# Optimization experiments

Hardware: AMD Instinct MI355X
Metric: run time of the kernel (lower is better)

## Reference

```python
import jax, jax.numpy as jnp
from jax import lax
import numpy as np

B, T, H, IN = 64, 2048, 256, 1


def setup_inputs() -> dict:
    key = jax.random.key(0)
    ks = jax.random.split(key, 12)
    s = 1.0 / np.sqrt(H)  # torch LSTM init scale (use normal*s for simplicity)
    return {
        "x": jax.random.normal(ks[0], (B, T, IN), jnp.float32),
        "Wih0": jax.random.normal(ks[1], (4 * H, IN), jnp.float32) * s,
        "Whh0": jax.random.normal(ks[2], (4 * H, H), jnp.float32) * s,
        "bih0": jax.random.normal(ks[3], (4 * H,), jnp.float32) * s,
        "bhh0": jax.random.normal(ks[4], (4 * H,), jnp.float32) * s,
        "Wih1": jax.random.normal(ks[5], (4 * H, H), jnp.float32) * s,
        "Whh1": jax.random.normal(ks[6], (4 * H, H), jnp.float32) * s,
        "bih1": jax.random.normal(ks[7], (4 * H,), jnp.float32) * s,
        "bhh1": jax.random.normal(ks[8], (4 * H,), jnp.float32) * s,
        "fc_w": jax.random.normal(ks[9], (1, H), jnp.float32) * s,
        "fc_b": jax.random.normal(ks[10], (1,), jnp.float32) * s,
    }


def _lstm_layer(x, Wih, Whh, bih, bhh):
    # x: [B, T, D_in] -> h sequence [B, T, H]; torch gate order (i, f, g, o)
    Bb = x.shape[0]
    Hh = Whh.shape[1]
    # precompute input contribution for all timesteps: [B, T, 4H]
    xg = jnp.einsum('btd,gd->btg', x, Wih) + bih + bhh

    def step(carry, xt):
        h, c = carry
        g = xt + h @ Whh.T  # [B, 4H]
        i, f, gg, o = jnp.split(g, 4, axis=-1)
        i = jax.nn.sigmoid(i)
        f = jax.nn.sigmoid(f)
        gg = jnp.tanh(gg)
        o = jax.nn.sigmoid(o)
        c = f * c + i * gg
        h = o * jnp.tanh(c)
        return (h, c), h

    h0 = jnp.zeros((Bb, Hh), x.dtype)
    c0 = jnp.zeros((Bb, Hh), x.dtype)
    (_, _), hs = lax.scan(step, (h0, c0), jnp.swapaxes(xg, 0, 1))  # hs: [T, B, H]
    return jnp.swapaxes(hs, 0, 1)


def reference(x, Wih0, Whh0, bih0, bhh0, Wih1, Whh1, bih1, bhh1, fc_w, fc_b):
    h1 = _lstm_layer(x, Wih0, Whh0, bih0, bhh0)   # [B, T, H]
    h2 = _lstm_layer(h1, Wih1, Whh1, bih1, bhh1)  # [B, T, H]
    out = jnp.einsum('bth,oh->bto', h2, fc_w) + fc_b  # [B, T, 1]
    return out
```

## Files before the change

kernel.cpp:

```cpp
#include <hip/hip_runtime.h>

#define TT 2048
#define NTHR 512
#define NWG 64

#define ABORT_O 0
#define FL_O    1024
#define H0_O    16384
#define H1_O    (16384 + 2*65536)
#define WS_TOTAL (16384 + 4*65536)

#define A0_HI    0
#define A0_LO    16384
#define AIH_HI   0
#define AIH_LO   16384
#define AHH_HI   32768
#define AHH_LO   49152
#define FWL_O    65536
#define HSH_O    65600
#define SMEM_BYTES 67648

typedef __bf16 bf16;
typedef __bf16 bf16x8 __attribute__((ext_vector_type(8)));
typedef float f32x4 __attribute__((ext_vector_type(4)));
typedef unsigned int u32;
typedef u32 u32x4 __attribute__((ext_vector_type(4)));
typedef unsigned short u16;

__device__ __forceinline__ f32x4 MFMA(bf16x8 a, bf16x8 b, f32x4 c) {
  return __builtin_amdgcn_mfma_f32_16x16x32_bf16(a, b, c, 0, 0, 0);
}
__device__ __forceinline__ float sigf(float v) { return 1.0f / (1.0f + __expf(-v)); }
__device__ __forceinline__ float tanhfast(float x) {
  float e = __expf(2.0f * x);
  return 1.0f - 2.0f / (e + 1.0f);
}
__device__ __forceinline__ u16 bfbits(float f) { return __builtin_bit_cast(u16, (bf16)f); }

__device__ __forceinline__ bf16x8 ld16d(const void* p) {
  u32x4 v;
  asm volatile("global_load_dwordx4 %0, %1, off sc0 sc1" : "=v"(v) : "v"(p));
  return __builtin_bit_cast(bf16x8, v);
}
__device__ __forceinline__ void wait_all_loads() {
  asm volatile("s_waitcnt vmcnt(0)" ::: "memory");
  __builtin_amdgcn_sched_barrier(0);
}
__device__ __forceinline__ void st16d(void* p, u16 h) {
  u32 v = h;
  asm volatile("global_store_short %0, %1, off sc0 sc1" :: "v"(p), "v"(v) : "memory");
}
__device__ __forceinline__ void st32_deep(u32* p, u32 v) {
  asm volatile("global_store_dword %0, %1, off sc0 sc1" :: "v"(p), "v"(v) : "memory");
}
__device__ __forceinline__ u32 ld_deep(const u32* p) {
  u32 v;
  asm volatile("global_load_dword %0, %1, off sc0 sc1\n\ts_waitcnt vmcnt(0)"
               : "=v"(v) : "v"(p) : "memory");
  return v;
}

__device__ __forceinline__ void wait_barrier(const u32* flags, u32 need, u32* abortp) {
  const int lane = threadIdx.x & 63;
  const u32* p = flags + lane * 32;
  int it = 0;
  for (;;) {
    u32 v = ld_deep(p);
    if (__all((int)(v >= need))) break;
    if (((++it) & 63) == 0) {
      u32 ab = ld_deep(abortp);
      if (__any((int)(ab != 0))) break;
      if (it >= (1 << 16)) { if (lane == 0) st32_deep(abortp, 1u); break; }
    }
  }
}

extern "C" __global__ __launch_bounds__(NTHR)
void lstm_persist(const float* __restrict__ x,
                  const float* __restrict__ Wih0, const float* __restrict__ Whh0,
                  const float* __restrict__ bih0, const float* __restrict__ bhh0,
                  const float* __restrict__ Wih1, const float* __restrict__ Whh1,
                  const float* __restrict__ bih1, const float* __restrict__ bhh1,
                  const float* __restrict__ fcw, const float* __restrict__ fcb,
                  float* __restrict__ out, char* __restrict__ ws)
{
  extern __shared__ char smem[];
  const int tid  = threadIdx.x;
  const int slot = blockIdx.x;
  const bool isL1 = slot >= 32;
  const int sl = isL1 ? slot - 32 : slot;

  u32* abortp = (u32*)(ws + ABORT_O);
  u32* flags  = (u32*)(ws + FL_O);

  const int w = tid >> 6, l = tid & 63, lr = l & 15, lk = l >> 4;
  const int rowb = (w & 1) * 16;
  const int colb = (w >> 1) * 16;
  const int b  = colb + lr;
  const int i  = (w & 1) * 4 + lk;
  const int gd = sl * 8 + i;

  if (!isL1) {
    bf16x8* Ahi = (bf16x8*)(smem + A0_HI);
    bf16x8* Alo = (bf16x8*)(smem + A0_LO);
    for (int idx = tid; idx < 1024; idx += NTHR) {
      int r = idx >> 5, kb = idx & 31;
      int grow = (r & 3) * 256 + sl * 8 + (r >> 2);
      const float* src = Whh0 + grow * 256 + kb * 8;
      bf16x8 hi, lo;
#pragma unroll
      for (int e = 0; e < 8; e++) { float v = src[e]; bf16 h = (bf16)v; hi[e] = h; lo[e] = (bf16)(v - (float)h); }
      Ahi[kb * 32 + r] = hi;  Alo[kb * 32 + r] = lo;
    }
  } else {
    bf16x8* AihH = (bf16x8*)(smem + AIH_HI);
    bf16x8* AihL = (bf16x8*)(smem + AIH_LO);
    bf16x8* AhhH = (bf16x8*)(smem + AHH_HI);
    bf16x8* AhhL = (bf16x8*)(smem + AHH_LO);
    for (int idx = tid; idx < 1024; idx += NTHR) {
      int r = idx >> 5, kb = idx & 31;
      int grow = (r & 3) * 256 + sl * 8 + (r >> 2);
      {
        const float* src = Wih1 + grow * 256 + kb * 8;
        bf16x8 hi, lo;
#pragma unroll
        for (int e = 0; e < 8; e++) { float v = src[e]; bf16 h = (bf16)v; hi[e] = h; lo[e] = (bf16)(v - (float)h); }
        AihH[kb * 32 + r] = hi;  AihL[kb * 32 + r] = lo;
      }
      {
        const float* src = Whh1 + grow * 256 + kb * 8;
        bf16x8 hi, lo;
#pragma unroll
        for (int e = 0; e < 8; e++) { float v = src[e]; bf16 h = (bf16)v; hi[e] = h; lo[e] = (bf16)(v - (float)h); }
        AhhH[kb * 32 + r] = hi;  AhhL[kb * 32 + r] = lo;
      }
    }
    if (tid < 8) ((float*)(smem + FWL_O))[tid] = fcw[sl * 8 + tid];
  }

  float wib_r[4], bias_r[4];
#pragma unroll
  for (int g = 0; g < 4; g++) {
    if (!isL1) { wib_r[g] = Wih0[g * 256 + gd]; bias_r[g] = bih0[g * 256 + gd] + bhh0[g * 256 + gd]; }
    else       { wib_r[g] = 0.0f;               bias_r[g] = bih1[g * 256 + gd] + bhh1[g * 256 + gd]; }
  }
  float creg = 0.0f;
  const float fb = fcb[0];
  __syncthreads();

  for (int t = 0; t <= TT; ++t) {
    if (t > 0) {
      if (tid < 64) wait_barrier(flags, (u32)t, abortp);
      __syncthreads();
    }

    if (!isL1) {
      if (t < TT) {
        const char* hp = ws + H0_O + (size_t)((t - 1) & 1) * 65536;
        bf16x8 bh[8], bl[8];
#pragma unroll
        for (int ks = 0; ks < 8; ks++) {
          int kb = ks * 4 + lk;
          const char* p = hp + (size_t)(kb * 64 + b) * 16;
          bh[ks] = ld16d(p);
          bl[ks] = ld16d(p + 32768);
        }
        float xv = x[(size_t)b * TT + t];
        wait_all_loads();

        bf16x8* Ahi = (bf16x8*)(smem + A0_HI);
        bf16x8* Alo = (bf16x8*)(smem + A0_LO);
        f32x4 acc = {0.f, 0.f, 0.f, 0.f};
#pragma unroll
        for (int ks = 0; ks < 8; ks++) {
          int kb = ks * 4 + lk;
          bf16x8 ah = Ahi[kb * 32 + rowb + lr];
          bf16x8 al = Alo[kb * 32 + rowb + lr];
          acc = MFMA(ah, bh[ks], acc);
          acc = MFMA(ah, bl[ks], acc);
          acc = MFMA(al, bh[ks], acc);
        }
        float pi = acc[0] + wib_r[0] * xv + bias_r[0];
        float pf = acc[1] + wib_r[1] * xv + bias_r[1];
        float pg = acc[2] + wib_r[2] * xv + bias_r[2];
        float po = acc[3] + wib_r[3] * xv + bias_r[3];
        float c = sigf(pf) * creg + sigf(pi) * tanhfast(pg);
        creg = c;
        float h = sigf(po) * tanhfast(c);
        u16 hb = bfbits(h);
        u16 lb = bfbits(h - (float)(bf16)h);
        char* wp = ws + H0_O + (size_t)(t & 1) * 65536 + (size_t)(sl * 64 + b) * 16 + i * 2;
        st16d(wp, hb);
        st16d(wp + 32768, lb);
      }
    } else {
      if (t >= 1) {
        const char* h0p = ws + H0_O + (size_t)((t - 1) & 1) * 65536;
        const char* h1p = ws + H1_O + (size_t)(t & 1) * 65536;
        bf16x8 b0h[8], b0l[8], b1h[8], b1l[8];
#pragma unroll
        for (int ks = 0; ks < 8; ks++) {
          int kb = ks * 4 + lk;
          const char* p0 = h0p + (size_t)(kb * 64 + b) * 16;
          const char* p1 = h1p + (size_t)(kb * 64 + b) * 16;
          b0h[ks] = ld16d(p0);  b0l[ks] = ld16d(p0 + 32768);
          b1h[ks] = ld16d(p1);  b1l[ks] = ld16d(p1 + 32768);
        }
        wait_all_loads();

        bf16x8* AihH = (bf16x8*)(smem + AIH_HI);
        bf16x8* AihL = (bf16x8*)(smem + AIH_LO);
        bf16x8* AhhH = (bf16x8*)(smem + AHH_HI);
        bf16x8* AhhL = (bf16x8*)(smem + AHH_LO);
        f32x4 acc = {0.f, 0.f, 0.f, 0.f};
#pragma unroll
        for (int ks = 0; ks < 8; ks++) {
          int kb = ks * 4 + lk;
          bf16x8 aih = AihH[kb * 32 + rowb + lr];
          bf16x8 ail = AihL[kb * 32 + rowb + lr];
          bf16x8 ahh = AhhH[kb * 32 + rowb + lr];
          bf16x8 ahl = AhhL[kb * 32 + rowb + lr];
          acc = MFMA(aih, b0h[ks], acc);
          acc = MFMA(aih, b0l[ks], acc);
          acc = MFMA(ail, b0h[ks], acc);
          acc = MFMA(ahh, b1h[ks], acc);
          acc = MFMA(ahh, b1l[ks], acc);
          acc = MFMA(ahl, b1h[ks], acc);
        }
        float pi = acc[0] + bias_r[0];
        float pf = acc[1] + bias_r[1];
        float pg = acc[2] + bias_r[2];
        float po = acc[3] + bias_r[3];
        float c = sigf(pf) * creg + sigf(pi) * tanhfast(pg);
        creg = c;
        float h = sigf(po) * tanhfast(c);
        u16 hb = bfbits(h);
        u16 lb = bfbits(h - (float)(bf16)h);
        char* wp = ws + H1_O + (size_t)((t - 1) & 1) * 65536 + (size_t)(sl * 64 + b) * 16 + i * 2;
        st16d(wp, hb);
        st16d(wp + 32768, lb);
        ((float*)(smem + HSH_O))[i * 64 + b] = h;
      }
    }

    asm volatile("s_waitcnt vmcnt(0)" ::: "memory");
    __syncthreads();
    if (tid == 0 && t < TT)
      st32_deep(flags + slot * 32, (u32)(t + 1));

    if (isL1 && t >= 1 && tid >= 64 && tid < 128) {
      const float* hsh = (const float*)(smem + HSH_O);
      const float* fwl = (const float*)(smem + FWL_O);
      int bb = tid - 64;
      float acc = 0.0f;
#pragma unroll
      for (int d = 0; d < 8; d++) acc += fwl[d] * hsh[d * 64 + bb];
      if (sl == 0) acc += fb;
      atomicAdd(out + (size_t)bb * TT + (t - 1), acc);
    }
  }
}

extern "C" void kernel_launch(void* const* d_in, const int* in_sizes, int n_in,
                              void* d_out, int out_size, void* d_ws, size_t ws_size,
                              hipStream_t stream) {
  (void)in_sizes; (void)n_in; (void)ws_size;
  hipFuncSetAttribute((const void*)lstm_persist,
                      hipFuncAttributeMaxDynamicSharedMemorySize, SMEM_BYTES);
  hipMemsetAsync(d_ws, 0, WS_TOTAL, stream);
  hipMemsetAsync(d_out, 0, (size_t)out_size * sizeof(float), stream);
  lstm_persist<<<dim3(NWG), dim3(NTHR), SMEM_BYTES, stream>>>(
      (const float*)d_in[0],
      (const float*)d_in[1], (const float*)d_in[2],
      (const float*)d_in[3], (const float*)d_in[4],
      (const float*)d_in[5], (const float*)d_in[6],
      (const float*)d_in[7], (const float*)d_in[8],
      (const float*)d_in[9], (const float*)d_in[10],
      (float*)d_out, (char*)d_ws);
}
```

Measured before the change: 9.152 ms.

## Exchange hidden state as fp32 and split to bf16 hi/lo on the consumer side

Producers now write h as a single 32-bit float store instead of two 16-bit stores of bf16 hi/lo parts. Consumers load two dwordx4 per fragment and rebuild the hi/lo bf16 split in registers before the MFMAs. Barrier flags are packed contiguously instead of padded 128 bytes apart, and MFMAs on the all-zero initial state are skipped. This halves the store count and turns sub-word stores into dword stores, at the price of extra conversion ALU work on the critical path and possible contention on the shared flag cache line.

```diff
diff --git a/kernel.cpp b/kernel.cpp
--- a/kernel.cpp
+++ b/kernel.cpp
@@ -5,7 +5,7 @@
 #define NWG 64
 
 #define ABORT_O 0
-#define FL_O    1024
+#define FL_O    256
 #define H0_O    16384
 #define H1_O    (16384 + 2*65536)
 #define WS_TOTAL (16384 + 4*65536)
@@ -35,20 +35,15 @@
   float e = __expf(2.0f * x);
   return 1.0f - 2.0f / (e + 1.0f);
 }
-__device__ __forceinline__ u16 bfbits(float f) { return __builtin_bit_cast(u16, (bf16)f); }
-
-__device__ __forceinline__ bf16x8 ld16d(const void* p) {
+
+__device__ __forceinline__ u32x4 ld16d(const void* p) {
   u32x4 v;
   asm volatile("global_load_dwordx4 %0, %1, off sc0 sc1" : "=v"(v) : "v"(p));
-  return __builtin_bit_cast(bf16x8, v);
+  return v;
 }
 __device__ __forceinline__ void wait_all_loads() {
   asm volatile("s_waitcnt vmcnt(0)" ::: "memory");
   __builtin_amdgcn_sched_barrier(0);
-}
-__device__ __forceinline__ void st16d(void* p, u16 h) {
-  u32 v = h;
-  asm volatile("global_store_short %0, %1, off sc0 sc1" :: "v"(p), "v"(v) : "memory");
 }
 __device__ __forceinline__ void st32_deep(u32* p, u32 v) {
   asm volatile("global_store_dword %0, %1, off sc0 sc1" :: "v"(p), "v"(v) : "memory");
@@ -60,9 +55,36 @@
   return v;
 }
 
+__device__ __forceinline__ u32 cv_hi(u32 w0, u32 w1) {
+  float f0 = __builtin_bit_cast(float, w0);
+  float f1 = __builtin_bit_cast(float, w1);
+  u16 h0 = __builtin_bit_cast(u16, (bf16)f0);
+  u16 h1 = __builtin_bit_cast(u16, (bf16)f1);
+  return (u32)h0 | ((u32)h1 << 16);
+}
+__device__ __forceinline__ u32 cv_lo(u32 w0, u32 w1) {
+  float f0 = __builtin_bit_cast(float, w0);
+  float f1 = __builtin_bit_cast(float, w1);
+  float r0 = f0 - (float)((bf16)f0);
+  float r1 = f1 - (float)((bf16)f1);
+  u16 l0 = __builtin_bit_cast(u16, (bf16)r0);
+  u16 l1 = __builtin_bit_cast(u16, (bf16)r1);
+  return (u32)l0 | ((u32)l1 << 16);
+}
+
+__device__ __forceinline__ void mk_frags(u32x4 qa, u32x4 qb, bf16x8& bh, bf16x8& bl) {
+  u32x4 ph, pl;
+  ph[0] = cv_hi(qa[0], qa[1]);  pl[0] = cv_lo(qa[0], qa[1]);
+  ph[1] = cv_hi(qa[2], qa[3]);  pl[1] = cv_lo(qa[2], qa[3]);
+  ph[2] = cv_hi(qb[0], qb[1]);  pl[2] = cv_lo(qb[0], qb[1]);
+  ph[3] = cv_hi(qb[2], qb[3]);  pl[3] = cv_lo(qb[2], qb[3]);
+  bh = __builtin_bit_cast(bf16x8, ph);
+  bl = __builtin_bit_cast(bf16x8, pl);
+}
+
 __device__ __forceinline__ void wait_barrier(const u32* flags, u32 need, u32* abortp) {
   const int lane = threadIdx.x & 63;
-  const u32* p = flags + lane * 32;
+  const u32* p = flags + lane;
   int it = 0;
   for (;;) {
     u32 v = ld_deep(p);
@@ -70,7 +92,7 @@
     if (((++it) & 63) == 0) {
       u32 ab = ld_deep(abortp);
       if (__any((int)(ab != 0))) break;
-      if (it >= (1 << 16)) { if (lane == 0) st32_deep(abortp, 1u); break; }
+      if (it >= (1 << 16)) { if (lane == 0) st32_deep((u32*)abortp, 1u); break; }
     }
   }
 }
@@ -88,7 +110,7 @@
   const int tid  = threadIdx.x;
   const int slot = blockIdx.x;
   const bool isL1 = slot >= 32;
-  const int sl = isL1 ? slot - 32 : slot;
+  const int sl = slot & 31;
 
   u32* abortp = (u32*)(ws + ABORT_O);
   u32* flags  = (u32*)(ws + FL_O);
@@ -99,6 +121,7 @@
   const int b  = colb + lr;
   const int i  = (w & 1) * 4 + lk;
   const int gd = sl * 8 + i;
+  const u32 hwi = (u32)(((sl * 2 + (i >> 2)) * 64 + b) * 4 + (i & 3));
 
   if (!isL1) {
     bf16x8* Ahi = (bf16x8*)(smem + A0_HI);
@@ -157,28 +180,30 @@
     if (!isL1) {
       if (t < TT) {
         const char* hp = ws + H0_O + (size_t)((t - 1) & 1) * 65536;
-        bf16x8 bh[8], bl[8];
+        u32x4 qa[8], qb[8];
 #pragma unroll
         for (int ks = 0; ks < 8; ks++) {
           int kb = ks * 4 + lk;
-          const char* p = hp + (size_t)(kb * 64 + b) * 16;
-          bh[ks] = ld16d(p);
-          bl[ks] = ld16d(p + 32768);
+          qa[ks] = ld16d(hp + (size_t)((kb * 2) * 64 + b) * 16);
+          qb[ks] = ld16d(hp + (size_t)((kb * 2 + 1) * 64 + b) * 16);
         }
         float xv = x[(size_t)b * TT + t];
         wait_all_loads();
 
-        bf16x8* Ahi = (bf16x8*)(smem + A0_HI);
-        bf16x8* Alo = (bf16x8*)(smem + A0_LO);
+        const bf16x8* Ahi = (const bf16x8*)(smem + A0_HI);
+        const bf16x8* Alo = (const bf16x8*)(smem + A0_LO);
         f32x4 acc = {0.f, 0.f, 0.f, 0.f};
-#pragma unroll
-        for (int ks = 0; ks < 8; ks++) {
-          int kb = ks * 4 + lk;
-          bf16x8 ah = Ahi[kb * 32 + rowb + lr];
-          bf16x8 al = Alo[kb * 32 + rowb + lr];
-          acc = MFMA(ah, bh[ks], acc);
-          acc = MFMA(ah, bl[ks], acc);
-          acc = MFMA(al, bh[ks], acc);
+        if (t > 0) {
+#pragma unroll
+          for (int ks = 0; ks < 8; ks++) {
+            bf16x8 bh, bl;
+            mk_frags(qa[ks], qb[ks], bh, bl);
+            bf16x8 ah = Ahi[(ks * 4 + lk) * 32 + rowb + lr];
+            bf16x8 al = Alo[(ks * 4 + lk) * 32 + rowb + lr];
+            acc = MFMA(ah, bh, acc);
+            acc = MFMA(ah, bl, acc);
+            acc = MFMA(al, bh, acc);
+          }
         }
         float pi = acc[0] + wib_r[0] * xv + bias_r[0];
         float pf = acc[1] + wib_r[1] * xv + bias_r[1];
@@ -187,45 +212,48 @@
         float c = sigf(pf) * creg + sigf(pi) * tanhfast(pg);
         creg = c;
         float h = sigf(po) * tanhfast(c);
-        u16 hb = bfbits(h);
-        u16 lb = bfbits(h - (float)(bf16)h);
-        char* wp = ws + H0_O + (size_t)(t & 1) * 65536 + (size_t)(sl * 64 + b) * 16 + i * 2;
-        st16d(wp, hb);
-        st16d(wp + 32768, lb);
+        st32_deep((u32*)(ws + H0_O + (size_t)(t & 1) * 65536) + hwi,
+                  __builtin_bit_cast(u32, h));
       }
     } else {
       if (t >= 1) {
         const char* h0p = ws + H0_O + (size_t)((t - 1) & 1) * 65536;
         const char* h1p = ws + H1_O + (size_t)(t & 1) * 65536;
-        bf16x8 b0h[8], b0l[8], b1h[8], b1l[8];
+        u32x4 qa0[8], qb0[8], qa1[8], qb1[8];
 #pragma unroll
         for (int ks = 0; ks < 8; ks++) {
           int kb = ks * 4 + lk;
-          const char* p0 = h0p + (size_t)(kb * 64 + b) * 16;
-          const char* p1 = h1p + (size_t)(kb * 64 + b) * 16;
-          b0h[ks] = ld16d(p0);  b0l[ks] = ld16d(p0 + 32768);
-          b1h[ks] = ld16d(p1);  b1l[ks] = ld16d(p1 + 32768);
+          qa0[ks] = ld16d(h0p + (size_t)((kb * 2) * 64 + b) * 16);
+          qb0[ks] = ld16d(h0p + (size_t)((kb * 2 + 1) * 64 + b) * 16);
+          qa1[ks] = ld16d(h1p + (size_t)((kb * 2) * 64 + b) * 16);
+          qb1[ks] = ld16d(h1p + (size_t)((kb * 2 + 1) * 64 + b) * 16);
         }
         wait_all_loads();
 
-        bf16x8* AihH = (bf16x8*)(smem + AIH_HI);
-        bf16x8* AihL = (bf16x8*)(smem + AIH_LO);
-        bf16x8* AhhH = (bf16x8*)(smem + AHH_HI);
-        bf16x8* AhhL = (bf16x8*)(smem + AHH_LO);
+        const bf16x8* AihH = (const bf16x8*)(smem + AIH_HI);
+        const bf16x8* AihL = (const bf16x8*)(smem + AIH_LO);
+        const bf16x8* AhhH = (const bf16x8*)(smem + AHH_HI);
+        const bf16x8* AhhL = (const bf16x8*)(smem + AHH_LO);
         f32x4 acc = {0.f, 0.f, 0.f, 0.f};
 #pragma unroll
         for (int ks = 0; ks < 8; ks++) {
           int kb = ks * 4 + lk;
+          bf16x8 bh, bl;
+          mk_frags(qa0[ks], qb0[ks], bh, bl);
           bf16x8 aih = AihH[kb * 32 + rowb + lr];
           bf16x8 ail = AihL[kb * 32 + rowb + lr];
-          bf16x8 ahh = AhhH[kb * 32 + rowb + lr];
-          bf16x8 ahl = AhhL[kb * 32 + rowb + lr];
-          acc = MFMA(aih, b0h[ks], acc);
-          acc = MFMA(aih, b0l[ks], acc);
-          acc = MFMA(ail, b0h[ks], acc);
-          acc = MFMA(ahh, b1h[ks], acc);
-          acc = MFMA(ahh, b1l[ks], acc);
-          acc = MFMA(ahl, b1h[ks], acc);
+          acc = MFMA(aih, bh, acc);
+          acc = MFMA(aih, bl, acc);
+          acc = MFMA(ail, bh, acc);
+          if (t >= 2) {
+            bf16x8 ch, cl;
+            mk_frags(qa1[ks], qb1[ks], ch, cl);
+            bf16x8 ahh = AhhH[kb * 32 + rowb + lr];
+            bf16x8 ahl = AhhL[kb * 32 + rowb + lr];
+            acc = MFMA(ahh, ch, acc);
+            acc = MFMA(ahh, cl, acc);
+            acc = MFMA(ahl, ch, acc);
+          }
         }
         float pi = acc[0] + bias_r[0];
         float pf = acc[1] + bias_r[1];
@@ -234,11 +262,8 @@
         float c = sigf(pf) * creg + sigf(pi) * tanhfast(pg);
         creg = c;
         float h = sigf(po) * tanhfast(c);
-        u16 hb = bfbits(h);
-        u16 lb = bfbits(h - (float)(bf16)h);
-        char* wp = ws + H1_O + (size_t)((t - 1) & 1) * 65536 + (size_t)(sl * 64 + b) * 16 + i * 2;
-        st16d(wp, hb);
-        st16d(wp + 32768, lb);
+        st32_deep((u32*)(ws + H1_O + (size_t)((t - 1) & 1) * 65536) + hwi,
+                  __builtin_bit_cast(u32, h));
         ((float*)(smem + HSH_O))[i * 64 + b] = h;
       }
     }
@@ -246,7 +271,7 @@
     asm volatile("s_waitcnt vmcnt(0)" ::: "memory");
     __syncthreads();
     if (tid == 0 && t < TT)
-      st32_deep(flags + slot * 32, (u32)(t + 1));
+      st32_deep(&flags[slot], (u32)(t + 1));
 
     if (isL1 && t >= 1 && tid >= 64 && tid < 128) {
       const float* hsh = (const float*)(smem + HSH_O);
@@ -265,10 +290,10 @@
                               void* d_out, int out_size, void* d_ws, size_t ws_size,
                               hipStream_t stream) {
   (void)in_sizes; (void)n_in; (void)ws_size;
-  hipFuncSetAttribute((const void*)lstm_persist,
-                      hipFuncAttributeMaxDynamicSharedMemorySize, SMEM_BYTES);
-  hipMemsetAsync(d_ws, 0, WS_TOTAL, stream);
-  hipMemsetAsync(d_out, 0, (size_t)out_size * sizeof(float), stream);
+  (void)hipFuncSetAttribute((const void*)lstm_persist,
+                            hipFuncAttributeMaxDynamicSharedMemorySize, SMEM_BYTES);
+  (void)hipMemsetAsync(d_ws, 0, WS_TOTAL, stream);
+  (void)hipMemsetAsync(d_out, 0, (size_t)out_size * sizeof(float), stream);
   lstm_persist<<<dim3(NWG), dim3(NTHR), SMEM_BYTES, stream>>>(
       (const float*)d_in[0],
       (const float*)d_in[1], (const float*)d_in[2],
```

New measurement: 15.85 ms. +73.1%, slower.

## Loosen layer-0 barrier dependency on layer-1 with 4-deep h0 ring buffer

Applied to the files above, without the earlier changes.

Layer-0 workgroups no longer wait on layer-1 progress for the current step. They only require layer-1 flags from two steps back, and h0 now sits in a 4-slot ring so it cannot be overwritten before layer 1 consumes it. This lets layer 0 run ahead and cuts the stalls caused by the lockstep global barrier between the two layers. It also skips MFMAs on known-zero initial hidden states at t=0 for layer 0 and t=1 for layer 1, at the cost of more workspace and a looser ordering argument that must hold for correctness.

```diff
diff --git a/kernel.cpp b/kernel.cpp
--- a/kernel.cpp
+++ b/kernel.cpp
@@ -7,8 +7,8 @@
 #define ABORT_O 0
 #define FL_O    1024
 #define H0_O    16384
-#define H1_O    (16384 + 2*65536)
-#define WS_TOTAL (16384 + 4*65536)
+#define H1_O    (16384 + 4*65536)
+#define WS_TOTAL (16384 + 4*65536 + 2*65536)
 
 #define A0_HI    0
 #define A0_LO    16384
@@ -60,8 +60,10 @@
   return v;
 }
 
-__device__ __forceinline__ void wait_barrier(const u32* flags, u32 need, u32* abortp) {
+__device__ __forceinline__ void wait_barrier(const u32* flags, u32 need_lo, u32 need_hi,
+                                             u32* abortp) {
   const int lane = threadIdx.x & 63;
+  const u32 need = (lane < 32) ? need_lo : need_hi;
   const u32* p = flags + lane * 32;
   int it = 0;
   for (;;) {
@@ -88,7 +90,7 @@
   const int tid  = threadIdx.x;
   const int slot = blockIdx.x;
   const bool isL1 = slot >= 32;
-  const int sl = isL1 ? slot - 32 : slot;
+  const int sl = slot & 31;
 
   u32* abortp = (u32*)(ws + ABORT_O);
   u32* flags  = (u32*)(ws + FL_O);
@@ -150,13 +152,16 @@
 
   for (int t = 0; t <= TT; ++t) {
     if (t > 0) {
-      if (tid < 64) wait_barrier(flags, (u32)t, abortp);
+      if (tid < 64) {
+        u32 need_hi = isL1 ? (u32)t : (t >= 2 ? (u32)(t - 2) : 0u);
+        wait_barrier(flags, (u32)t, need_hi, abortp);
+      }
       __syncthreads();
     }
 
     if (!isL1) {
       if (t < TT) {
-        const char* hp = ws + H0_O + (size_t)((t - 1) & 1) * 65536;
+        const char* hp = ws + H0_O + (size_t)((t + 3) & 3) * 65536;
         bf16x8 bh[8], bl[8];
 #pragma unroll
         for (int ks = 0; ks < 8; ks++) {
@@ -168,17 +173,19 @@
         float xv = x[(size_t)b * TT + t];
         wait_all_loads();
 
-        bf16x8* Ahi = (bf16x8*)(smem + A0_HI);
-        bf16x8* Alo = (bf16x8*)(smem + A0_LO);
+        const bf16x8* Ahi = (const bf16x8*)(smem + A0_HI);
+        const bf16x8* Alo = (const bf16x8*)(smem + A0_LO);
         f32x4 acc = {0.f, 0.f, 0.f, 0.f};
-#pragma unroll
-        for (int ks = 0; ks < 8; ks++) {
-          int kb = ks * 4 + lk;
-          bf16x8 ah = Ahi[kb * 32 + rowb + lr];
-          bf16x8 al = Alo[kb * 32 + rowb + lr];
-          acc = MFMA(ah, bh[ks], acc);
-          acc = MFMA(ah, bl[ks], acc);
-          acc = MFMA(al, bh[ks], acc);
+        if (t > 0) {
+#pragma unroll
+          for (int ks = 0; ks < 8; ks++) {
+            int kb = ks * 4 + lk;
+            bf16x8 ah = Ahi[kb * 32 + rowb + lr];
+            bf16x8 al = Alo[kb * 32 + rowb + lr];
+            acc = MFMA(ah, bh[ks], acc);
+            acc = MFMA(ah, bl[ks], acc);
+            acc = MFMA(al, bh[ks], acc);
+          }
         }
         float pi = acc[0] + wib_r[0] * xv + bias_r[0];
         float pf = acc[1] + wib_r[1] * xv + bias_r[1];
@@ -189,13 +196,13 @@
         float h = sigf(po) * tanhfast(c);
         u16 hb = bfbits(h);
         u16 lb = bfbits(h - (float)(bf16)h);
-        char* wp = ws + H0_O + (size_t)(t & 1) * 65536 + (size_t)(sl * 64 + b) * 16 + i * 2;
+        char* wp = ws + H0_O + (size_t)(t & 3) * 65536 + (size_t)(sl * 64 + b) * 16 + i * 2;
         st16d(wp, hb);
         st16d(wp + 32768, lb);
       }
     } else {
       if (t >= 1) {
-        const char* h0p = ws + H0_O + (size_t)((t - 1) & 1) * 65536;
+        const char* h0p = ws + H0_O + (size_t)((t + 3) & 3) * 65536;
         const char* h1p = ws + H1_O + (size_t)(t & 1) * 65536;
         bf16x8 b0h[8], b0l[8], b1h[8], b1l[8];
 #pragma unroll
@@ -208,24 +215,26 @@
         }
         wait_all_loads();
 
-        bf16x8* AihH = (bf16x8*)(smem + AIH_HI);
-        bf16x8* AihL = (bf16x8*)(smem + AIH_LO);
-        bf16x8* AhhH = (bf16x8*)(smem + AHH_HI);
-        bf16x8* AhhL = (bf16x8*)(smem + AHH_LO);
+        const bf16x8* AihH = (const bf16x8*)(smem + AIH_HI);
+        const bf16x8* AihL = (const bf16x8*)(smem + AIH_LO);
+        const bf16x8* AhhH = (const bf16x8*)(smem + AHH_HI);
+        const bf16x8* AhhL = (const bf16x8*)(smem + AHH_LO);
         f32x4 acc = {0.f, 0.f, 0.f, 0.f};
 #pragma unroll
         for (int ks = 0; ks < 8; ks++) {
           int kb = ks * 4 + lk;
           bf16x8 aih = AihH[kb * 32 + rowb + lr];
           bf16x8 ail = AihL[kb * 32 + rowb + lr];
-          bf16x8 ahh = AhhH[kb * 32 + rowb + lr];
-          bf16x8 ahl = AhhL[kb * 32 + rowb + lr];
           acc = MFMA(aih, b0h[ks], acc);
           acc = MFMA(aih, b0l[ks], acc);
           acc = MFMA(ail, b0h[ks], acc);
-          acc = MFMA(ahh, b1h[ks], acc);
-          acc = MFMA(ahh, b1l[ks], acc);
-          acc = MFMA(ahl, b1h[ks], acc);
+          if (t >= 2) {
+            bf16x8 ahh = AhhH[kb * 32 + rowb + lr];
+            bf16x8 ahl = AhhL[kb * 32 + rowb + lr];
+            acc = MFMA(ahh, b1h[ks], acc);
+            acc = MFMA(ahh, b1l[ks], acc);
+            acc = MFMA(ahl, b1h[ks], acc);
+          }
         }
         float pi = acc[0] + bias_r[0];
         float pf = acc[1] + bias_r[1];
@@ -265,10 +274,10 @@
                               void* d_out, int out_size, void* d_ws, size_t ws_size,
                               hipStream_t stream) {
   (void)in_sizes; (void)n_in; (void)ws_size;
-  hipFuncSetAttribute((const void*)lstm_persist,
-                      hipFuncAttributeMaxDynamicSharedMemorySize, SMEM_BYTES);
-  hipMemsetAsync(d_ws, 0, WS_TOTAL, stream);
-  hipMemsetAsync(d_out, 0, (size_t)out_size * sizeof(float), stream);
+  (void)hipFuncSetAttribute((const void*)lstm_persist,
+                            hipFuncAttributeMaxDynamicSharedMemorySize, SMEM_BYTES);
+  (void)hipMemsetAsync(d_ws, 0, WS_TOTAL, stream);
+  (void)hipMemsetAsync(d_out, 0, (size_t)out_size * sizeof(float), stream);
   lstm_persist<<<dim3(NWG), dim3(NTHR), SMEM_BYTES, stream>>>(
       (const float*)d_in[0],
       (const float*)d_in[1], (const float*)d_in[2],
```

Result: no change. 9.296 ms (+1.6%).
